# Optimization experiments

Measured on AMD Instinct MI355X. Metric: run time of the kernel, lower is better.

## Reference

```python
import jax, jax.numpy as jnp
import numpy as np

B, N, C = 16, 8192, 64
NPOINT, NSAMPLE = 1024, 32
RADIUS = 0.1


def setup_inputs() -> dict:
    key = jax.random.key(0)
    ks = jax.random.split(key, 6)
    xyz = jax.random.uniform(ks[0], (B, N, 3), jnp.float32)          # points in unit cube
    features = jax.random.normal(ks[1], (B, C, N), jnp.float32)
    W1 = jax.random.normal(ks[2], (64, 67), jnp.float32) * 0.1
    b1 = jnp.zeros((64,), jnp.float32)
    W2 = jax.random.normal(ks[3], (64, 64), jnp.float32) * 0.1
    b2 = jnp.zeros((64,), jnp.float32)
    W3 = jax.random.normal(ks[4], (128, 64), jnp.float32) * 0.1
    b3 = jnp.zeros((128,), jnp.float32)
    return dict(xyz=xyz, features=features, W1=W1, b1=b1, W2=W2, b2=b2, W3=W3, b3=b3)


def _fps(pts, npoint):
    """Furthest point sampling on a single cloud pts:(N,3) -> (npoint,) int32 indices."""
    n = pts.shape[0]
    def step(carry, _):
        dist, far = carry
        d = jnp.sum((pts - pts[far]) ** 2, axis=-1)   # (N,)
        dist = jnp.minimum(dist, d)
        return (dist, jnp.argmax(dist).astype(jnp.int32)), far
    init = (jnp.full((n,), 1e10, pts.dtype), jnp.int32(0))
    _, idx = jax.lax.scan(step, init, None, length=npoint)
    return idx


def reference(xyz, features, W1, b1, W2, b2, W3, b3):
    n = xyz.shape[1]
    # --- furthest point sample + gather centroids ---
    idx = jax.lax.stop_gradient(jax.vmap(lambda p: _fps(p, NPOINT))(xyz))   # (B,npoint)
    new_xyz = jnp.take_along_axis(xyz, idx[:, :, None], axis=1)             # (B,npoint,3)
    # --- ball query: first NSAMPLE indices with dist < r, pad with first hit (0 if none) ---
    d2 = jnp.sum((new_xyz[:, :, None, :] - xyz[:, None, :, :]) ** 2, axis=-1)  # (B,npoint,N)
    cand = jnp.where(d2 < RADIUS ** 2, jnp.arange(n, dtype=jnp.int32), n)
    sm = -jax.lax.top_k(-cand, NSAMPLE)[0]                                   # smallest NSAMPLE, ascending
    first = sm[..., :1]
    first = jnp.where(first == n, 0, first)
    gidx = jax.lax.stop_gradient(jnp.where(sm == n, first, sm))              # (B,npoint,nsample)
    # --- group: relative xyz + gathered features, concat on channel dim ---
    gxyz = jax.vmap(lambda p, i: p[i])(xyz, gidx)                            # (B,npoint,nsample,3)
    gxyz = (gxyz - new_xyz[:, :, None, :]).transpose(0, 3, 1, 2)             # (B,3,npoint,nsample)
    gfeat = jax.vmap(lambda f, i: f[:, i])(features, gidx)                   # (B,C,npoint,nsample)
    h = jnp.concatenate([gxyz, gfeat], axis=1)                               # (B,3+C,npoint,nsample)
    # --- shared MLP (1x1 conv + ReLU per layer) ---
    for W, b in ((W1, b1), (W2, b2), (W3, b3)):
        h = jax.nn.relu(jnp.einsum('oc,bcps->bops', W, h) + b[None, :, None, None])
    # --- max-pool over neighbors ---
    new_features = jnp.max(h, axis=-1)                                       # (B,128,npoint)
    return new_xyz, new_features
```

## Files before the change

kernel.cpp:

```cpp
#include <hip/hip_runtime.h>

#define BATCH   16
#define NPTS    8192
#define NCH     64
#define NPOINT  1024
#define NSAMPLE 32
#define R2 0.01f

__device__ inline unsigned long long shfl_xor_u64(unsigned long long x, int m) {
    int lo = (int)(unsigned)(x & 0xffffffffull);
    int hi = (int)(unsigned)(x >> 32);
    lo = __shfl_xor(lo, m, 64);
    hi = __shfl_xor(hi, m, 64);
    return ((unsigned long long)(unsigned)hi << 32) | (unsigned)lo;
}

__global__ __launch_bounds__(256, 1) void fps_tr_kernel(const float* __restrict__ xyz,
                                                        float* __restrict__ new_xyz,
                                                        const float* __restrict__ feat,
                                                        float* __restrict__ feat_t) {
    __shared__ float s_mem[NPTS * 3];
    __shared__ unsigned long long s_red[2][4];
    const int t = threadIdx.x;

    if (blockIdx.x >= BATCH) {
        float (*tile)[65] = (float (*)[65])s_mem;
        const int bidx = blockIdx.x - BATCH;
        const int b  = bidx >> 7;
        const int n0 = (bidx & 127) << 6;
        const int i  = t & 63, c0 = t >> 6;
        const float* src = feat + (size_t)b * NCH * NPTS;
#pragma unroll
        for (int r = 0; r < 16; ++r) {
            int c = c0 + r * 4;
            tile[c][i] = src[(size_t)c * NPTS + n0 + i];
        }
        __syncthreads();
        const int cc = t & 63, i0 = t >> 6;
        float* dst = feat_t + ((size_t)b * NPTS + n0) * NCH;
#pragma unroll
        for (int r = 0; r < 16; ++r) {
            int ii = i0 + r * 4;
            dst[(size_t)ii * NCH + cc] = tile[cc][ii];
        }
        return;
    }

    const int b = blockIdx.x;
    const float* g = xyz + (size_t)b * NPTS * 3;
    for (int i = t; i < NPTS * 3; i += 256) s_mem[i] = g[i];
    __syncthreads();

    float px[32], py[32], pz[32], dist[32];
#pragma unroll
    for (int k = 0; k < 32; ++k) {
        const int p = t + (k << 8);
        px[k] = s_mem[3 * p + 0];
        py[k] = s_mem[3 * p + 1];
        pz[k] = s_mem[3 * p + 2];
        dist[k] = 1e10f;
    }

    float fx = s_mem[0], fy = s_mem[1], fz = s_mem[2];
    const int wave = t >> 6;

    for (int it = 0; it < NPOINT; ++it) {
        if (t == 0) {
            float* nx = new_xyz + ((size_t)b * NPOINT + it) * 3;
            nx[0] = fx; nx[1] = fy; nx[2] = fz;
        }
        float bestv = -1.0f; int bestk = 0;
#pragma unroll
        for (int k = 0; k < 32; ++k) {
            float dx = __fsub_rn(px[k], fx);
            float dy = __fsub_rn(py[k], fy);
            float dz = __fsub_rn(pz[k], fz);
            float d  = __fadd_rn(__fadd_rn(__fmul_rn(dx, dx), __fmul_rn(dy, dy)),
                                 __fmul_rn(dz, dz));
            float nd = fminf(dist[k], d);
            dist[k] = nd;
            if (nd > bestv) { bestv = nd; bestk = k; }
        }
        const int besti = t + (bestk << 8);
        unsigned long long key =
            ((unsigned long long)__float_as_uint(bestv) << 32) | (unsigned)(~besti);
#pragma unroll
        for (int m = 1; m < 64; m <<= 1) {
            unsigned long long o = shfl_xor_u64(key, m);
            if (o > key) key = o;
        }
        const int par = it & 1;
        if ((t & 63) == 0) s_red[par][wave] = key;
        __syncthreads();
        unsigned long long kk = s_red[par][0];
        unsigned long long k1 = s_red[par][1];
        unsigned long long k2 = s_red[par][2];
        unsigned long long k3 = s_red[par][3];
        if (k1 > kk) kk = k1;
        if (k2 > kk) kk = k2;
        if (k3 > kk) kk = k3;
        const int far = (int)(~(unsigned)kk);
        fx = s_mem[3 * far + 0];
        fy = s_mem[3 * far + 1];
        fz = s_mem[3 * far + 2];
    }
}

__global__ __launch_bounds__(256) void ballquery_kernel(const float* __restrict__ xyz,
                                                        const float* __restrict__ new_xyz,
                                                        int* __restrict__ gidx) {
    const int gw   = (blockIdx.x * 256 + threadIdx.x) >> 6;
    const int lane = threadIdx.x & 63;
    const int b = gw >> 10;
    const float* nx = new_xyz + (size_t)gw * 3;
    const float cx = nx[0], cy = nx[1], cz = nx[2];
    const float* pts = xyz + (size_t)b * NPTS * 3;
    int* out = gidx + (size_t)gw * NSAMPLE;

    int cnt = 0;
    int first = 0;
    for (int j0 = 0; j0 < NPTS; j0 += 64) {
        const int j = j0 + lane;
        float x = pts[3 * j], y = pts[3 * j + 1], z = pts[3 * j + 2];
        float dx = __fsub_rn(x, cx), dy = __fsub_rn(y, cy), dz = __fsub_rn(z, cz);
        float d2 = __fadd_rn(__fadd_rn(__fmul_rn(dx, dx), __fmul_rn(dy, dy)),
                             __fmul_rn(dz, dz));
        const bool pred = d2 < R2;
        const unsigned long long mask = __ballot(pred);
        if (cnt == 0 && mask) first = j0 + (int)(__ffsll((unsigned long long)mask) - 1);
        if (pred) {
            int slot = cnt + (int)__popcll(mask & ((1ull << lane) - 1ull));
            if (slot < NSAMPLE) out[slot] = j;
        }
        cnt += (int)__popcll(mask);
        if (cnt >= NSAMPLE) break;
    }
    if (cnt < NSAMPLE) {
        if (lane >= cnt && lane < NSAMPLE) out[lane] = first;
    }
}

__global__ __launch_bounds__(256) void mlp_kernel(const float* __restrict__ xyz,
                                                  const float* __restrict__ feat_t,
                                                  const int* __restrict__ gidx,
                                                  const float* __restrict__ new_xyz,
                                                  const float* __restrict__ W1,
                                                  const float* __restrict__ b1,
                                                  const float* __restrict__ W2,
                                                  const float* __restrict__ b2,
                                                  const float* __restrict__ W3,
                                                  const float* __restrict__ b3,
                                                  float* __restrict__ out_feat) {
    __shared__ float sw[128 * 64];
    __shared__ float sb1[64], sb2[64], sb3[128];
    const int t = threadIdx.x;

    for (int i = t; i < 64 * 67; i += 256) sw[(i / 67) * 68 + (i % 67)] = W1[i];
    if (t < 64) { sw[t * 68 + 67] = 0.0f; sb1[t] = b1[t]; sb2[t] = b2[t]; }
    if (t < 128) sb3[t] = b3[t];

    const int ci = t >> 5, s = t & 31;
    const int pg = blockIdx.x * 8 + ci;
    const int b  = pg >> 10;
    const int p  = pg & 1023;
    const int gi = gidx[(size_t)pg * NSAMPLE + s];

    const float* nx = new_xyz + (size_t)pg * 3;
    const float* pp = xyz + ((size_t)b * NPTS + gi) * 3;
    float h[68];
    h[0] = pp[0] - nx[0];
    h[1] = pp[1] - nx[1];
    h[2] = pp[2] - nx[2];
    const float4* fp = (const float4*)(feat_t + ((size_t)b * NPTS + gi) * NCH);
#pragma unroll
    for (int q = 0; q < 16; ++q) {
        float4 v = fp[q];
        h[3 + 4 * q] = v.x; h[4 + 4 * q] = v.y; h[5 + 4 * q] = v.z; h[6 + 4 * q] = v.w;
    }
    h[67] = 0.0f;
    __syncthreads();

    float h1[64];
#pragma unroll
    for (int o = 0; o < 64; ++o) {
        const float4* wr = (const float4*)(&sw[o * 68]);
        float a0 = 0.f, a1 = 0.f, a2 = 0.f, a3 = 0.f;
#pragma unroll
        for (int q = 0; q < 17; ++q) {
            float4 w = wr[q];
            a0 = fmaf(w.x, h[4 * q + 0], a0);
            a1 = fmaf(w.y, h[4 * q + 1], a1);
            a2 = fmaf(w.z, h[4 * q + 2], a2);
            a3 = fmaf(w.w, h[4 * q + 3], a3);
        }
        h1[o] = fmaxf((a0 + a1) + (a2 + a3) + sb1[o], 0.0f);
    }

    __syncthreads();
    for (int i = t; i < 64 * 64; i += 256) sw[i] = W2[i];
    __syncthreads();

    float h2[64];
#pragma unroll
    for (int o = 0; o < 64; ++o) {
        const float4* wr = (const float4*)(&sw[o * 64]);
        float a0 = 0.f, a1 = 0.f, a2 = 0.f, a3 = 0.f;
#pragma unroll
        for (int q = 0; q < 16; ++q) {
            float4 w = wr[q];
            a0 = fmaf(w.x, h1[4 * q + 0], a0);
            a1 = fmaf(w.y, h1[4 * q + 1], a1);
            a2 = fmaf(w.z, h1[4 * q + 2], a2);
            a3 = fmaf(w.w, h1[4 * q + 3], a3);
        }
        h2[o] = fmaxf((a0 + a1) + (a2 + a3) + sb2[o], 0.0f);
    }

    __syncthreads();
    for (int i = t; i < 128 * 64; i += 256) sw[i] = W3[i];
    __syncthreads();

    float* outp = out_feat + ((size_t)b * 128) * NPOINT + p;
#pragma unroll
    for (int o = 0; o < 128; ++o) {
        const float4* wr = (const float4*)(&sw[o * 64]);
        float a0 = 0.f, a1 = 0.f, a2 = 0.f, a3 = 0.f;
#pragma unroll
        for (int q = 0; q < 16; ++q) {
            float4 w = wr[q];
            a0 = fmaf(w.x, h2[4 * q + 0], a0);
            a1 = fmaf(w.y, h2[4 * q + 1], a1);
            a2 = fmaf(w.z, h2[4 * q + 2], a2);
            a3 = fmaf(w.w, h2[4 * q + 3], a3);
        }
        float acc = fmaxf((a0 + a1) + (a2 + a3) + sb3[o], 0.0f);
#pragma unroll
        for (int m = 1; m < 32; m <<= 1) acc = fmaxf(acc, __shfl_xor(acc, m, 64));
        if (s == 0) outp[(size_t)o * NPOINT] = acc;
    }
}

extern "C" void kernel_launch(void* const* d_in, const int* in_sizes, int n_in,
                              void* d_out, int out_size, void* d_ws, size_t ws_size,
                              hipStream_t stream) {
    const float* xyz  = (const float*)d_in[0];
    const float* feat = (const float*)d_in[1];
    const float* W1   = (const float*)d_in[2];
    const float* b1   = (const float*)d_in[3];
    const float* W2   = (const float*)d_in[4];
    const float* b2   = (const float*)d_in[5];
    const float* W3   = (const float*)d_in[6];
    const float* b3   = (const float*)d_in[7];

    float* new_xyz  = (float*)d_out;
    float* out_feat = (float*)d_out + (size_t)BATCH * NPOINT * 3;

    int* gidx = (int*)d_ws;
    size_t gidx_bytes = (size_t)BATCH * NPOINT * NSAMPLE * sizeof(int);
    gidx_bytes = (gidx_bytes + 255) & ~(size_t)255;
    float* feat_t = (float*)((char*)d_ws + gidx_bytes);

    hipLaunchKernelGGL(fps_tr_kernel, dim3(BATCH + BATCH * (NPTS / 64)), dim3(256), 0, stream,
                       xyz, new_xyz, feat, feat_t);
    hipLaunchKernelGGL(ballquery_kernel, dim3(BATCH * NPOINT / 4), dim3(256), 0, stream,
                       xyz, new_xyz, gidx);
    hipLaunchKernelGGL(mlp_kernel, dim3(BATCH * NPOINT / 8), dim3(256), 0, stream,
                       xyz, feat_t, gidx, new_xyz,
                       W1, b1, W2, b2, W3, b3, out_feat);
}
```

Before: 1.780 ms.

## Fuse FPS, ball query and MLP into one persistent kernel with progress flags

Merges the three kernels into a single persistent launch. Sixteen blocks run FPS while 240 worker blocks first transpose features, then spin on per-batch progress counters so they can run ball query and the MLP on centroids as soon as they are produced. This overlaps the serial FPS with the downstream work and keeps ball-query indices in shared memory instead of a global buffer. The cost is that correctness depends on every block being co-resident, since spin-waiting blocks would deadlock otherwise. The workers also spend time polling with sleeps.

After: 2.469 ms. +38.7%, slower.

```diff
diff --git a/kernel.cpp b/kernel.cpp
--- a/kernel.cpp
+++ b/kernel.cpp
@@ -5,7 +5,9 @@
 #define NCH     64
 #define NPOINT  1024
 #define NSAMPLE 32
-#define R2 0.01f
+#define R2      0.01f
+#define NWORK   240
+#define NGROUPS 2048
 
 __device__ inline unsigned long long shfl_xor_u64(unsigned long long x, int m) {
     int lo = (int)(unsigned)(x & 0xffffffffull);
@@ -15,25 +17,115 @@
     return ((unsigned long long)(unsigned)hi << 32) | (unsigned)lo;
 }
 
-__global__ __launch_bounds__(256, 1) void fps_tr_kernel(const float* __restrict__ xyz,
-                                                        float* __restrict__ new_xyz,
-                                                        const float* __restrict__ feat,
-                                                        float* __restrict__ feat_t) {
-    __shared__ float s_mem[NPTS * 3];
-    __shared__ unsigned long long s_red[2][4];
+struct FpsShared {
+    float pts[NPTS * 3];
+    unsigned long long red[2][4];
+};
+struct WkShared {
+    float tile[64][65];
+    float w1[64 * 68];
+    float w2[64 * 64];
+    float w3[128 * 64];
+    float b1s[64], b2s[64], b3s[128];
+    int   gidx[8][NSAMPLE];
+};
+
+__global__ void init_kernel(int* prog, int* cnt) {
+    if (threadIdx.x < BATCH) prog[threadIdx.x] = 0;
+    if (threadIdx.x == BATCH) *cnt = 0;
+}
+
+__global__ __launch_bounds__(256, 1) void fused_kernel(const float* __restrict__ xyz,
+                                                       const float* __restrict__ feat,
+                                                       const float* __restrict__ W1,
+                                                       const float* __restrict__ b1,
+                                                       const float* __restrict__ W2,
+                                                       const float* __restrict__ b2,
+                                                       const float* __restrict__ W3,
+                                                       const float* __restrict__ b3,
+                                                       float* __restrict__ new_xyz,
+                                                       float* __restrict__ out_feat,
+                                                       float* __restrict__ feat_t,
+                                                       int* prog, int* cnt) {
+    __shared__ union { FpsShared fps; WkShared wk; } U;
     const int t = threadIdx.x;
 
-    if (blockIdx.x >= BATCH) {
-        float (*tile)[65] = (float (*)[65])s_mem;
-        const int bidx = blockIdx.x - BATCH;
-        const int b  = bidx >> 7;
-        const int n0 = (bidx & 127) << 6;
+    if (blockIdx.x < BATCH) {
+        const int b = blockIdx.x;
+        const float* g = xyz + (size_t)b * NPTS * 3;
+        for (int i = t; i < NPTS * 3; i += 256) U.fps.pts[i] = g[i];
+        __syncthreads();
+
+        float px[32], py[32], pz[32], dist[32];
+#pragma unroll
+        for (int k = 0; k < 32; ++k) {
+            const int p = t + (k << 8);
+            px[k] = U.fps.pts[3 * p + 0];
+            py[k] = U.fps.pts[3 * p + 1];
+            pz[k] = U.fps.pts[3 * p + 2];
+            dist[k] = 1e10f;
+        }
+
+        float fx = U.fps.pts[0], fy = U.fps.pts[1], fz = U.fps.pts[2];
+        const int wave = t >> 6;
+
+        for (int it = 0; it < NPOINT; ++it) {
+            if (t == 0) {
+                float* nx = new_xyz + ((size_t)b * NPOINT + it) * 3;
+                nx[0] = fx; nx[1] = fy; nx[2] = fz;
+                if (((it + 1) & 15) == 0)
+                    __hip_atomic_store(&prog[b], it + 1, __ATOMIC_RELEASE,
+                                       __HIP_MEMORY_SCOPE_AGENT);
+            }
+            float bestv = -1.0f; int bestk = 0;
+#pragma unroll
+            for (int k = 0; k < 32; ++k) {
+                float dx = __fsub_rn(px[k], fx);
+                float dy = __fsub_rn(py[k], fy);
+                float dz = __fsub_rn(pz[k], fz);
+                float d  = __fadd_rn(__fadd_rn(__fmul_rn(dx, dx), __fmul_rn(dy, dy)),
+                                     __fmul_rn(dz, dz));
+                float nd = fminf(dist[k], d);
+                dist[k] = nd;
+                if (nd > bestv) { bestv = nd; bestk = k; }
+            }
+            const int besti = t + (bestk << 8);
+            unsigned long long key =
+                ((unsigned long long)__float_as_uint(bestv) << 32) | (unsigned)(~besti);
+#pragma unroll
+            for (int m = 1; m < 64; m <<= 1) {
+                unsigned long long o = shfl_xor_u64(key, m);
+                if (o > key) key = o;
+            }
+            const int par = it & 1;
+            if ((t & 63) == 0) U.fps.red[par][wave] = key;
+            __syncthreads();
+            unsigned long long kk = U.fps.red[par][0];
+            unsigned long long k1 = U.fps.red[par][1];
+            unsigned long long k2 = U.fps.red[par][2];
+            unsigned long long k3 = U.fps.red[par][3];
+            if (k1 > kk) kk = k1;
+            if (k2 > kk) kk = k2;
+            if (k3 > kk) kk = k3;
+            const int far = (int)(~(unsigned)kk);
+            fx = U.fps.pts[3 * far + 0];
+            fy = U.fps.pts[3 * far + 1];
+            fz = U.fps.pts[3 * far + 2];
+        }
+        return;
+    }
+
+    const int wid = blockIdx.x - BATCH;
+
+    for (int tid = wid; tid < BATCH * (NPTS / 64); tid += NWORK) {
+        const int b  = tid >> 7;
+        const int n0 = (tid & 127) << 6;
         const int i  = t & 63, c0 = t >> 6;
         const float* src = feat + (size_t)b * NCH * NPTS;
 #pragma unroll
         for (int r = 0; r < 16; ++r) {
             int c = c0 + r * 4;
-            tile[c][i] = src[(size_t)c * NPTS + n0 + i];
+            U.wk.tile[c][i] = src[(size_t)c * NPTS + n0 + i];
         }
         __syncthreads();
         const int cc = t & 63, i0 = t >> 6;
@@ -41,202 +133,132 @@
 #pragma unroll
         for (int r = 0; r < 16; ++r) {
             int ii = i0 + r * 4;
-            dst[(size_t)ii * NCH + cc] = tile[cc][ii];
-        }
-        return;
-    }
-
-    const int b = blockIdx.x;
-    const float* g = xyz + (size_t)b * NPTS * 3;
-    for (int i = t; i < NPTS * 3; i += 256) s_mem[i] = g[i];
+            dst[(size_t)ii * NCH + cc] = U.wk.tile[cc][ii];
+        }
+        __syncthreads();
+    }
+    if (t == 0)
+        __hip_atomic_fetch_add(cnt, 1, __ATOMIC_ACQ_REL, __HIP_MEMORY_SCOPE_AGENT);
+
+    for (int i = t; i < 64 * 67; i += 256) U.wk.w1[(i / 67) * 68 + (i % 67)] = W1[i];
+    if (t < 64) { U.wk.w1[t * 68 + 67] = 0.0f; U.wk.b1s[t] = b1[t]; U.wk.b2s[t] = b2[t]; }
+    if (t < 128) U.wk.b3s[t] = b3[t];
+    for (int i = t; i < 64 * 64; i += 256) U.wk.w2[i] = W2[i];
+    for (int i = t; i < 128 * 64; i += 256) U.wk.w3[i] = W3[i];
+
+    if (t == 0) {
+        while (__hip_atomic_load(cnt, __ATOMIC_ACQUIRE, __HIP_MEMORY_SCOPE_AGENT) < NWORK)
+            __builtin_amdgcn_s_sleep(8);
+    }
     __syncthreads();
 
-    float px[32], py[32], pz[32], dist[32];
-#pragma unroll
-    for (int k = 0; k < 32; ++k) {
-        const int p = t + (k << 8);
-        px[k] = s_mem[3 * p + 0];
-        py[k] = s_mem[3 * p + 1];
-        pz[k] = s_mem[3 * p + 2];
-        dist[k] = 1e10f;
-    }
-
-    float fx = s_mem[0], fy = s_mem[1], fz = s_mem[2];
-    const int wave = t >> 6;
-
-    for (int it = 0; it < NPOINT; ++it) {
+    const int wv = t >> 6, lane = t & 63;
+    for (int gidx_g = wid; gidx_g < NGROUPS; gidx_g += NWORK) {
+        const int b  = gidx_g >> 7;
+        const int p0 = (gidx_g & 127) << 3;
         if (t == 0) {
-            float* nx = new_xyz + ((size_t)b * NPOINT + it) * 3;
-            nx[0] = fx; nx[1] = fy; nx[2] = fz;
-        }
-        float bestv = -1.0f; int bestk = 0;
-#pragma unroll
-        for (int k = 0; k < 32; ++k) {
-            float dx = __fsub_rn(px[k], fx);
-            float dy = __fsub_rn(py[k], fy);
-            float dz = __fsub_rn(pz[k], fz);
-            float d  = __fadd_rn(__fadd_rn(__fmul_rn(dx, dx), __fmul_rn(dy, dy)),
-                                 __fmul_rn(dz, dz));
-            float nd = fminf(dist[k], d);
-            dist[k] = nd;
-            if (nd > bestv) { bestv = nd; bestk = k; }
-        }
-        const int besti = t + (bestk << 8);
-        unsigned long long key =
-            ((unsigned long long)__float_as_uint(bestv) << 32) | (unsigned)(~besti);
-#pragma unroll
-        for (int m = 1; m < 64; m <<= 1) {
-            unsigned long long o = shfl_xor_u64(key, m);
-            if (o > key) key = o;
-        }
-        const int par = it & 1;
-        if ((t & 63) == 0) s_red[par][wave] = key;
-        __syncthreads();
-        unsigned long long kk = s_red[par][0];
-        unsigned long long k1 = s_red[par][1];
-        unsigned long long k2 = s_red[par][2];
-        unsigned long long k3 = s_red[par][3];
-        if (k1 > kk) kk = k1;
-        if (k2 > kk) kk = k2;
-        if (k3 > kk) kk = k3;
-        const int far = (int)(~(unsigned)kk);
-        fx = s_mem[3 * far + 0];
-        fy = s_mem[3 * far + 1];
-        fz = s_mem[3 * far + 2];
-    }
-}
-
-__global__ __launch_bounds__(256) void ballquery_kernel(const float* __restrict__ xyz,
-                                                        const float* __restrict__ new_xyz,
-                                                        int* __restrict__ gidx) {
-    const int gw   = (blockIdx.x * 256 + threadIdx.x) >> 6;
-    const int lane = threadIdx.x & 63;
-    const int b = gw >> 10;
-    const float* nx = new_xyz + (size_t)gw * 3;
-    const float cx = nx[0], cy = nx[1], cz = nx[2];
-    const float* pts = xyz + (size_t)b * NPTS * 3;
-    int* out = gidx + (size_t)gw * NSAMPLE;
-
-    int cnt = 0;
-    int first = 0;
-    for (int j0 = 0; j0 < NPTS; j0 += 64) {
-        const int j = j0 + lane;
-        float x = pts[3 * j], y = pts[3 * j + 1], z = pts[3 * j + 2];
-        float dx = __fsub_rn(x, cx), dy = __fsub_rn(y, cy), dz = __fsub_rn(z, cz);
-        float d2 = __fadd_rn(__fadd_rn(__fmul_rn(dx, dx), __fmul_rn(dy, dy)),
-                             __fmul_rn(dz, dz));
-        const bool pred = d2 < R2;
-        const unsigned long long mask = __ballot(pred);
-        if (cnt == 0 && mask) first = j0 + (int)(__ffsll((unsigned long long)mask) - 1);
-        if (pred) {
-            int slot = cnt + (int)__popcll(mask & ((1ull << lane) - 1ull));
-            if (slot < NSAMPLE) out[slot] = j;
-        }
-        cnt += (int)__popcll(mask);
-        if (cnt >= NSAMPLE) break;
-    }
-    if (cnt < NSAMPLE) {
-        if (lane >= cnt && lane < NSAMPLE) out[lane] = first;
-    }
-}
-
-__global__ __launch_bounds__(256) void mlp_kernel(const float* __restrict__ xyz,
-                                                  const float* __restrict__ feat_t,
-                                                  const int* __restrict__ gidx,
-                                                  const float* __restrict__ new_xyz,
-                                                  const float* __restrict__ W1,
-                                                  const float* __restrict__ b1,
-                                                  const float* __restrict__ W2,
-                                                  const float* __restrict__ b2,
-                                                  const float* __restrict__ W3,
-                                                  const float* __restrict__ b3,
-                                                  float* __restrict__ out_feat) {
-    __shared__ float sw[128 * 64];
-    __shared__ float sb1[64], sb2[64], sb3[128];
-    const int t = threadIdx.x;
-
-    for (int i = t; i < 64 * 67; i += 256) sw[(i / 67) * 68 + (i % 67)] = W1[i];
-    if (t < 64) { sw[t * 68 + 67] = 0.0f; sb1[t] = b1[t]; sb2[t] = b2[t]; }
-    if (t < 128) sb3[t] = b3[t];
-
-    const int ci = t >> 5, s = t & 31;
-    const int pg = blockIdx.x * 8 + ci;
-    const int b  = pg >> 10;
-    const int p  = pg & 1023;
-    const int gi = gidx[(size_t)pg * NSAMPLE + s];
-
-    const float* nx = new_xyz + (size_t)pg * 3;
-    const float* pp = xyz + ((size_t)b * NPTS + gi) * 3;
-    float h[68];
-    h[0] = pp[0] - nx[0];
-    h[1] = pp[1] - nx[1];
-    h[2] = pp[2] - nx[2];
-    const float4* fp = (const float4*)(feat_t + ((size_t)b * NPTS + gi) * NCH);
-#pragma unroll
-    for (int q = 0; q < 16; ++q) {
-        float4 v = fp[q];
-        h[3 + 4 * q] = v.x; h[4 + 4 * q] = v.y; h[5 + 4 * q] = v.z; h[6 + 4 * q] = v.w;
-    }
-    h[67] = 0.0f;
-    __syncthreads();
-
-    float h1[64];
-#pragma unroll
-    for (int o = 0; o < 64; ++o) {
-        const float4* wr = (const float4*)(&sw[o * 68]);
-        float a0 = 0.f, a1 = 0.f, a2 = 0.f, a3 = 0.f;
-#pragma unroll
-        for (int q = 0; q < 17; ++q) {
-            float4 w = wr[q];
-            a0 = fmaf(w.x, h[4 * q + 0], a0);
-            a1 = fmaf(w.y, h[4 * q + 1], a1);
-            a2 = fmaf(w.z, h[4 * q + 2], a2);
-            a3 = fmaf(w.w, h[4 * q + 3], a3);
-        }
-        h1[o] = fmaxf((a0 + a1) + (a2 + a3) + sb1[o], 0.0f);
-    }
-
-    __syncthreads();
-    for (int i = t; i < 64 * 64; i += 256) sw[i] = W2[i];
-    __syncthreads();
-
-    float h2[64];
-#pragma unroll
-    for (int o = 0; o < 64; ++o) {
-        const float4* wr = (const float4*)(&sw[o * 64]);
-        float a0 = 0.f, a1 = 0.f, a2 = 0.f, a3 = 0.f;
-#pragma unroll
-        for (int q = 0; q < 16; ++q) {
-            float4 w = wr[q];
-            a0 = fmaf(w.x, h1[4 * q + 0], a0);
-            a1 = fmaf(w.y, h1[4 * q + 1], a1);
-            a2 = fmaf(w.z, h1[4 * q + 2], a2);
-            a3 = fmaf(w.w, h1[4 * q + 3], a3);
-        }
-        h2[o] = fmaxf((a0 + a1) + (a2 + a3) + sb2[o], 0.0f);
-    }
-
-    __syncthreads();
-    for (int i = t; i < 128 * 64; i += 256) sw[i] = W3[i];
-    __syncthreads();
-
-    float* outp = out_feat + ((size_t)b * 128) * NPOINT + p;
-#pragma unroll
-    for (int o = 0; o < 128; ++o) {
-        const float4* wr = (const float4*)(&sw[o * 64]);
-        float a0 = 0.f, a1 = 0.f, a2 = 0.f, a3 = 0.f;
-#pragma unroll
-        for (int q = 0; q < 16; ++q) {
-            float4 w = wr[q];
-            a0 = fmaf(w.x, h2[4 * q + 0], a0);
-            a1 = fmaf(w.y, h2[4 * q + 1], a1);
-            a2 = fmaf(w.z, h2[4 * q + 2], a2);
-            a3 = fmaf(w.w, h2[4 * q + 3], a3);
-        }
-        float acc = fmaxf((a0 + a1) + (a2 + a3) + sb3[o], 0.0f);
-#pragma unroll
-        for (int m = 1; m < 32; m <<= 1) acc = fmaxf(acc, __shfl_xor(acc, m, 64));
-        if (s == 0) outp[(size_t)o * NPOINT] = acc;
+            while (__hip_atomic_load(&prog[b], __ATOMIC_ACQUIRE,
+                                     __HIP_MEMORY_SCOPE_AGENT) < p0 + 8)
+                __builtin_amdgcn_s_sleep(8);
+        }
+        __syncthreads();
+
+        const float* pts = xyz + (size_t)b * NPTS * 3;
+        for (int q = 0; q < 2; ++q) {
+            const int ci = wv * 2 + q;
+            const float* nx = new_xyz + ((size_t)b * NPOINT + p0 + ci) * 3;
+            const float cx = nx[0], cy = nx[1], cz = nx[2];
+            int hits = 0, first = 0;
+            for (int j0 = 0; j0 < NPTS; j0 += 64) {
+                const int j = j0 + lane;
+                float x = pts[3 * j], y = pts[3 * j + 1], z = pts[3 * j + 2];
+                float dx = __fsub_rn(x, cx), dy = __fsub_rn(y, cy), dz = __fsub_rn(z, cz);
+                float d2 = __fadd_rn(__fadd_rn(__fmul_rn(dx, dx), __fmul_rn(dy, dy)),
+                                     __fmul_rn(dz, dz));
+                const bool pred = d2 < R2;
+                const unsigned long long mask = __ballot(pred);
+                if (hits == 0 && mask)
+                    first = j0 + (int)(__ffsll((unsigned long long)mask) - 1);
+                if (pred) {
+                    int slot = hits + (int)__popcll(mask & ((1ull << lane) - 1ull));
+                    if (slot < NSAMPLE) U.wk.gidx[ci][slot] = j;
+                }
+                hits += (int)__popcll(mask);
+                if (hits >= NSAMPLE) break;
+            }
+            if (hits < NSAMPLE && lane >= hits && lane < NSAMPLE)
+                U.wk.gidx[ci][lane] = first;
+        }
+        __syncthreads();
+
+        const int ci = t >> 5, s = t & 31;
+        const int p  = p0 + ci;
+        const int gi = U.wk.gidx[ci][s];
+        const float* nx = new_xyz + ((size_t)b * NPOINT + p) * 3;
+        const float* pp = xyz + ((size_t)b * NPTS + gi) * 3;
+        float h[68];
+        h[0] = pp[0] - nx[0];
+        h[1] = pp[1] - nx[1];
+        h[2] = pp[2] - nx[2];
+        const float4* fp = (const float4*)(feat_t + ((size_t)b * NPTS + gi) * NCH);
+#pragma unroll
+        for (int qq = 0; qq < 16; ++qq) {
+            float4 v = fp[qq];
+            h[3 + 4 * qq] = v.x; h[4 + 4 * qq] = v.y;
+            h[5 + 4 * qq] = v.z; h[6 + 4 * qq] = v.w;
+        }
+        h[67] = 0.0f;
+
+        float h1[64];
+#pragma unroll
+        for (int o = 0; o < 64; ++o) {
+            const float4* wr = (const float4*)(&U.wk.w1[o * 68]);
+            float a0 = 0.f, a1 = 0.f, a2 = 0.f, a3 = 0.f;
+#pragma unroll
+            for (int qq = 0; qq < 17; ++qq) {
+                float4 w = wr[qq];
+                a0 = fmaf(w.x, h[4 * qq + 0], a0);
+                a1 = fmaf(w.y, h[4 * qq + 1], a1);
+                a2 = fmaf(w.z, h[4 * qq + 2], a2);
+                a3 = fmaf(w.w, h[4 * qq + 3], a3);
+            }
+            h1[o] = fmaxf((a0 + a1) + (a2 + a3) + U.wk.b1s[o], 0.0f);
+        }
+
+        float h2[64];
+#pragma unroll
+        for (int o = 0; o < 64; ++o) {
+            const float4* wr = (const float4*)(&U.wk.w2[o * 64]);
+            float a0 = 0.f, a1 = 0.f, a2 = 0.f, a3 = 0.f;
+#pragma unroll
+            for (int qq = 0; qq < 16; ++qq) {
+                float4 w = wr[qq];
+                a0 = fmaf(w.x, h1[4 * qq + 0], a0);
+                a1 = fmaf(w.y, h1[4 * qq + 1], a1);
+                a2 = fmaf(w.z, h1[4 * qq + 2], a2);
+                a3 = fmaf(w.w, h1[4 * qq + 3], a3);
+            }
+            h2[o] = fmaxf((a0 + a1) + (a2 + a3) + U.wk.b2s[o], 0.0f);
+        }
+
+        float* outp = out_feat + ((size_t)b * 128) * NPOINT + p;
+#pragma unroll
+        for (int o = 0; o < 128; ++o) {
+            const float4* wr = (const float4*)(&U.wk.w3[o * 64]);
+            float a0 = 0.f, a1 = 0.f, a2 = 0.f, a3 = 0.f;
+#pragma unroll
+            for (int qq = 0; qq < 16; ++qq) {
+                float4 w = wr[qq];
+                a0 = fmaf(w.x, h2[4 * qq + 0], a0);
+                a1 = fmaf(w.y, h2[4 * qq + 1], a1);
+                a2 = fmaf(w.z, h2[4 * qq + 2], a2);
+                a3 = fmaf(w.w, h2[4 * qq + 3], a3);
+            }
+            float acc = fmaxf((a0 + a1) + (a2 + a3) + U.wk.b3s[o], 0.0f);
+#pragma unroll
+            for (int m = 1; m < 32; m <<= 1) acc = fmaxf(acc, __shfl_xor(acc, m, 64));
+            if (s == 0) outp[(size_t)o * NPOINT] = acc;
+        }
     }
 }
 
@@ -255,16 +277,12 @@
     float* new_xyz  = (float*)d_out;
     float* out_feat = (float*)d_out + (size_t)BATCH * NPOINT * 3;
 
-    int* gidx = (int*)d_ws;
-    size_t gidx_bytes = (size_t)BATCH * NPOINT * NSAMPLE * sizeof(int);
-    gidx_bytes = (gidx_bytes + 255) & ~(size_t)255;
-    float* feat_t = (float*)((char*)d_ws + gidx_bytes);
-
-    hipLaunchKernelGGL(fps_tr_kernel, dim3(BATCH + BATCH * (NPTS / 64)), dim3(256), 0, stream,
-                       xyz, new_xyz, feat, feat_t);
-    hipLaunchKernelGGL(ballquery_kernel, dim3(BATCH * NPOINT / 4), dim3(256), 0, stream,
-                       xyz, new_xyz, gidx);
-    hipLaunchKernelGGL(mlp_kernel, dim3(BATCH * NPOINT / 8), dim3(256), 0, stream,
-                       xyz, feat_t, gidx, new_xyz,
-                       W1, b1, W2, b2, W3, b3, out_feat);
-}
+    int*   prog   = (int*)d_ws;
+    int*   cnt    = prog + BATCH;
+    float* feat_t = (float*)((char*)d_ws + 256);
+
+    hipLaunchKernelGGL(init_kernel, dim3(1), dim3(64), 0, stream, prog, cnt);
+    hipLaunchKernelGGL(fused_kernel, dim3(BATCH + NWORK), dim3(256), 0, stream,
+                       xyz, feat, W1, b1, W2, b2, W3, b3,
+                       new_xyz, out_feat, feat_t, prog, cnt);
+}
```
